# Kernel optimization log

Hardware: AMD Instinct MI355X
Metric: run time of the kernel (lower is better)

## Reference

```python
import jax, jax.numpy as jnp
import numpy as np

N, E, D = 50000, 1200000, 64
NEG_SLOPE = 0.2  # PyG GATConv LeakyReLU slope
EPS_SM = 1e-16   # PyG softmax eps
EPS_LN = 1e-5


def _glorot(key, shape):
    fan = shape[0]
    return jax.random.normal(key, shape, jnp.float32) / np.float32(np.sqrt(fan))


def setup_inputs() -> dict:
    key = jax.random.key(0)
    ks = jax.random.split(key, 16)
    inp = {
        "x": jax.random.normal(ks[0], (N, D), jnp.float32),
        "edge_index": jax.random.randint(ks[1], (2, E), 0, N, dtype=jnp.int32),
        # layer 0: bipartite-style (-1,-1) GATConv -> separate src/dst projections
        "W_src0": _glorot(ks[2], (D, D)), "W_dst0": _glorot(ks[3], (D, D)),
        "a_src0": _glorot(ks[4], (D,)), "a_dst0": _glorot(ks[5], (D,)),
        "b0": jnp.zeros((D,), jnp.float32),
        "lin_W0": _glorot(ks[6], (D, D)), "lin_b0": jnp.zeros((D,), jnp.float32),
        # layers 1,2: int in_channels -> shared projection for src and dst
        "W1": _glorot(ks[7], (D, D)),
        "a_src1": _glorot(ks[8], (D,)), "a_dst1": _glorot(ks[9], (D,)),
        "b1": jnp.zeros((D,), jnp.float32),
        "lin_W1": _glorot(ks[10], (D, D)), "lin_b1": jnp.zeros((D,), jnp.float32),
        "W2": _glorot(ks[11], (D, D)),
        "a_src2": _glorot(ks[12], (D,)), "a_dst2": _glorot(ks[13], (D,)),
        "b2": jnp.zeros((D,), jnp.float32),
        "lin_W2": _glorot(ks[14], (D, D)), "lin_b2": jnp.zeros((D,), jnp.float32),
        "ln_w": jnp.ones((D,), jnp.float32), "ln_b": jnp.zeros((D,), jnp.float32),
        "proj_W": _glorot(ks[15], (D, 1)), "proj_b": jnp.zeros((1,), jnp.float32),
    }
    return inp


def _gat(x_src, x_dst, a_src, a_dst, bias, src, dst):
    # per-edge attention logit: a_src.x_j + a_dst.x_i, LeakyReLU
    alpha = (x_src * a_src).sum(-1)[src] + (x_dst * a_dst).sum(-1)[dst]  # [E]
    alpha = jnp.where(alpha >= 0, alpha, NEG_SLOPE * alpha)
    # segment softmax over edges sharing a destination node
    m = jax.ops.segment_max(alpha, dst, num_segments=N)
    m = jnp.where(jnp.isfinite(m), m, 0.0)  # empty segments -> -inf -> 0
    e = jnp.exp(alpha - m[dst])
    denom = jax.ops.segment_sum(e, dst, num_segments=N)
    w = e / (denom[dst] + EPS_SM)
    # weighted scatter-add aggregation
    return jax.ops.segment_sum(w[:, None] * x_src[src], dst, num_segments=N) + bias


def reference(x, edge_index,
              W_src0, W_dst0, a_src0, a_dst0, b0, lin_W0, lin_b0,
              W1, a_src1, a_dst1, b1, lin_W1, lin_b1,
              W2, a_src2, a_dst2, b2, lin_W2, lin_b2,
              ln_w, ln_b, proj_W, proj_b):
    src, dst = edge_index[0], edge_index[1]
    h = _gat(x @ W_src0, x @ W_dst0, a_src0, a_dst0, b0, src, dst) + x @ lin_W0 + lin_b0
    h = jax.nn.relu(h)
    hp = h @ W1
    h = _gat(hp, hp, a_src1, a_dst1, b1, src, dst) + h @ lin_W1 + lin_b1
    h = jax.nn.relu(h)
    hp = h @ W2
    h = _gat(hp, hp, a_src2, a_dst2, b2, src, dst) + h @ lin_W2 + lin_b2
    # PyG LayerNorm mode='graph': normalize over all nodes and channels
    mu = h.mean()
    var = h.var()
    h = (h - mu) * jax.lax.rsqrt(var + EPS_LN) * ln_w + ln_b
    return h @ proj_W + proj_b  # [N, 1]
```

## Files before the change

kernel.cpp:

```cpp
#include <hip/hip_runtime.h>
#include <hip/hip_bf16.h>

#define NN 50000
#define NE 1200000
#define D 64
#define NEG_SLOPE 0.2f
#define EPS_SM 1e-16f
#define EPS_LN 1e-5f
#define KMAX 4
#define PIPE 8
#define BSH 6
#define NBUK 782
#define BCAP 2048
#define BCAPSH 11
#define EPB 4096
#define NPB 293
#define PACKB 48
#define GEMM_BLOCKS 3125
#define GAT_BLOCKS 12500

typedef __attribute__((ext_vector_type(8))) short short8;
typedef __attribute__((ext_vector_type(4))) float float4v;

__device__ __forceinline__ float waveReduceSum(float v) {
    #pragma unroll
    for (int off = 32; off > 0; off >>= 1)
        v += __shfl_xor(v, off, 64);
    return v;
}
__device__ __forceinline__ float bflo(unsigned v) { return __uint_as_float(v << 16); }
__device__ __forceinline__ float bfhi(unsigned v) { return __uint_as_float(v & 0xffff0000u); }
__device__ __forceinline__ short f2bf_bits(float f) {
    __hip_bfloat16 b = __float2bfloat16(f);
    short v; __builtin_memcpy(&v, &b, 2);
    return v;
}

struct WP7 { const float* p[7]; };

__global__ __launch_bounds__(256) void prep(WP7 wp, unsigned short* __restrict__ wpk,
                                            const int* __restrict__ ei,
                                            int* __restrict__ bcur,
                                            int* __restrict__ pairs) {
    if (blockIdx.x >= NPB) {
        const int n = 7 * 4096;
        for (int idx = (blockIdx.x - NPB) * 256 + threadIdx.x; idx < n; idx += PACKB * 256) {
            const int j = idx & 7;
            const int lane = (idx >> 3) & 63;
            const int khtile = idx >> 9;
            const int kh = khtile & 1;
            const int tile = khtile >> 1;
            const int mat = tile >> 2;
            const int ch = (tile & 3) * 16 + (lane & 15);
            const int k = kh * 32 + (lane >> 4) * 8 + j;
            wpk[idx] = (unsigned short)f2bf_bits(wp.p[mat][k * D + ch]);
        }
        return;
    }
    __shared__ int h[NBUK];
    __shared__ int cur[NBUK];
    for (int i = threadIdx.x; i < NBUK; i += 256) h[i] = 0;
    __syncthreads();
    const int base = blockIdx.x * EPB;
    const int lim  = min(EPB, NE - base);
    for (int i = threadIdx.x; i < lim; i += 256)
        atomicAdd(&h[ei[NE + base + i] >> BSH], 1);
    __syncthreads();
    for (int i = threadIdx.x; i < NBUK; i += 256) {
        const int c = h[i];
        cur[i] = c ? atomicAdd(&bcur[i], c) : 0;
    }
    __syncthreads();
    for (int i = threadIdx.x; i < lim; i += 256) {
        const int s = ei[base + i];
        const int d = ei[NE + base + i];
        const int b = d >> BSH;
        const int pos = atomicAdd(&cur[b], 1);
        if (pos < BCAP) pairs[(b << BCAPSH) + pos] = s | ((d & 63) << 16);
    }
}

template <int NMATS>
__global__ __launch_bounds__(256) void gemm_mfma(
                          const float* __restrict__ hin,
                          const unsigned short* __restrict__ wpk,
                          const float* __restrict__ avs,
                          const float* __restrict__ avd,
                          const float* __restrict__ bgat,
                          const float* __restrict__ blin,
                          __hip_bfloat16* __restrict__ hp,
                          float* __restrict__ agg,
                          float* __restrict__ alpha_s,
                          float* __restrict__ alpha_d) {
    constexpr int NT   = NMATS * 4;
    constexpr int NTPW = NT / 4;
    __shared__ float ared[2][4][16];
    __shared__ unsigned short hpt[16][68];
    __shared__ float aggt[16][69];

    const int t   = threadIdx.x;
    const int nb0 = blockIdx.x * 16;

    const int w    = t >> 6;
    const int lane = t & 63;
    const int mrow = lane & 15;
    const int kq   = lane >> 4;

    const float* xrow = hin + (size_t)(nb0 + mrow) * D + kq * 8;
    short8 a[2];
    #pragma unroll
    for (int kh = 0; kh < 2; ++kh) {
        const float4 f0 = *(const float4*)(xrow + kh * 32);
        const float4 f1 = *(const float4*)(xrow + kh * 32 + 4);
        a[kh][0] = f2bf_bits(f0.x); a[kh][1] = f2bf_bits(f0.y);
        a[kh][2] = f2bf_bits(f0.z); a[kh][3] = f2bf_bits(f0.w);
        a[kh][4] = f2bf_bits(f1.x); a[kh][5] = f2bf_bits(f1.y);
        a[kh][6] = f2bf_bits(f1.z); a[kh][7] = f2bf_bits(f1.w);
    }

    float4v acc[NTPW];
    #pragma unroll
    for (int i = 0; i < NTPW; ++i) {
        const int tile = w * NTPW + i;
        const short8 b0 = *(const short8*)(wpk + ((size_t)(tile * 2 + 0) * 64 + lane) * 8);
        const short8 b1 = *(const short8*)(wpk + ((size_t)(tile * 2 + 1) * 64 + lane) * 8);
        float4v c = {0.f, 0.f, 0.f, 0.f};
        c = __builtin_amdgcn_mfma_f32_16x16x32_bf16(a[0], b0, c, 0, 0, 0);
        c = __builtin_amdgcn_mfma_f32_16x16x32_bf16(a[1], b1, c, 0, 0, 0);
        acc[i] = c;
    }

    float psr[4] = {0.f, 0.f, 0.f, 0.f};
    float pdr[4] = {0.f, 0.f, 0.f, 0.f};
    #pragma unroll
    for (int i = 0; i < NTPW; ++i) {
        const int tile = w * NTPW + i;
        const int mat  = tile >> 2;
        const int c64  = (tile & 3) * 16 + mrow;
        const float av_s = avs[c64], av_d = avd[c64];
        const float bias = blin[c64] + bgat[c64];
        #pragma unroll
        for (int r = 0; r < 4; ++r) {
            const int ln = kq * 4 + r;
            const float v = acc[i][r];
            if (mat == 0) {
                hpt[ln][c64] = (unsigned short)f2bf_bits(v);
                psr[r] += v * av_s;
                if (NMATS == 2) pdr[r] += v * av_d;
            } else if (NMATS == 3 && mat == 1) {
                pdr[r] += v * av_d;
            } else {
                aggt[ln][c64] = v + bias;
            }
        }
    }
    #pragma unroll
    for (int off = 1; off < 16; off <<= 1) {
        #pragma unroll
        for (int r = 0; r < 4; ++r) {
            psr[r] += __shfl_xor(psr[r], off, 64);
            pdr[r] += __shfl_xor(pdr[r], off, 64);
        }
    }
    if (mrow == 0) {
        #pragma unroll
        for (int r = 0; r < 4; ++r) {
            ared[0][w][kq * 4 + r] = psr[r];
            ared[1][w][kq * 4 + r] = pdr[r];
        }
    }
    __syncthreads();

    {
        const int row = t >> 4;
        const int c0  = (t & 15) * 4;
        const float4 av = { aggt[row][c0], aggt[row][c0 + 1],
                            aggt[row][c0 + 2], aggt[row][c0 + 3] };
        *(float4*)(agg + (size_t)(nb0 + row) * D + c0) = av;
    }
    if (t < 128) {
        const int hr = t >> 3;
        const int h0 = (t & 7) * 8;
        const unsigned* hrow = (const unsigned*)&hpt[hr][h0];
        const uint4 hv = { hrow[0], hrow[1], hrow[2], hrow[3] };
        *(uint4*)((unsigned short*)hp + (size_t)(nb0 + hr) * D + h0) = hv;
    }
    if (t < 16) {
        alpha_s[nb0 + t] = ared[0][0][t] + ared[0][1][t] + ared[0][2][t] + ared[0][3][t];
        alpha_d[nb0 + t] = ared[1][0][t] + ared[1][1][t] + ared[1][2][t] + ared[1][3][t];
    }
}

__global__ __launch_bounds__(256) void csr_finalize(const int* __restrict__ pairs,
                                                    const int* __restrict__ bcur,
                                                    int* __restrict__ cnt,
                                                    int* __restrict__ row_start,
                                                    int* __restrict__ csr_src) {
    __shared__ int ncnt[64];
    __shared__ int lsrc[BCAP];
    const int t = threadIdx.x;
    const int b = blockIdx.x;
    const int beg = b << BCAPSH;
    const int m = min(bcur[b], BCAP);
    const int nbase = b << BSH;
    if (t < 64) ncnt[t] = 0;
    __syncthreads();
    for (int i = t; i < m; i += 256)
        atomicAdd(&ncnt[pairs[beg + i] >> 16], 1);
    __syncthreads();
    if (t < 64) {
        const int v = ncnt[t];
        int inc = v;
        #pragma unroll
        for (int off = 1; off < 64; off <<= 1) {
            const int u = __shfl_up(inc, off, 64);
            if (t >= off) inc += u;
        }
        const int excl = inc - v;
        if (nbase + t < NN) {
            cnt[nbase + t] = v;
            row_start[nbase + t] = beg + excl;
        }
        ncnt[t] = excl;
    }
    __syncthreads();
    for (int i = t; i < m; i += 256) {
        const int p = pairs[beg + i];
        const int pos = atomicAdd(&ncnt[p >> 16], 1);
        lsrc[pos] = p & 0xffff;
    }
    __syncthreads();
    for (int i = t; i < m; i += 256)
        csr_src[beg + i] = lsrc[i];
}

template <bool DO_RELU, bool DO_STATS>
__global__ __launch_bounds__(256) void gat_node(
                         const int* __restrict__ csr_src,
                         const int* __restrict__ row_start,
                         const int* __restrict__ cnt,
                         const float* __restrict__ as,
                         const float* __restrict__ ad,
                         const __hip_bfloat16* __restrict__ hp,
                         float* __restrict__ agg,
                         float* __restrict__ partial) {
    __shared__ int2 esm[4][KMAX * 64];
    const int wv   = threadIdx.x >> 6;
    const int lane = threadIdx.x & 63;
    const int node = blockIdx.x * 4 + wv;
    const int snode = __builtin_amdgcn_readfirstlane(node);
    const int deg = cnt[snode];
    const int rs  = row_start[snode];
    const int half = lane >> 5;
    const int c2   = lane & 31;
    float2 acc = make_float2(0.f, 0.f);
    if (deg > 0) {
        const float ad_d = ad[snode];
        int   sr[KMAX];
        float ea[KMAX];
        float sum = 0.f;
        #pragma unroll
        for (int k = 0; k < KMAX; ++k) {
            const int j = k * 64 + lane;
            const bool valid = j < deg;
            const int s = valid ? __builtin_nontemporal_load(csr_src + rs + j) : 0;
            float a = valid ? (as[s] + ad_d) : 0.f;
            a = (a >= 0.f) ? a : NEG_SLOPE * a;
            float e = valid ? __expf(a) : 0.f;
            sr[k] = s;
            ea[k] = e;
            sum += e;
        }
        sum = waveReduceSum(sum);
        const float inv = 1.f / (sum + EPS_SM);
        #pragma unroll
        for (int k = 0; k < KMAX; ++k)
            esm[wv][k * 64 + lane] = make_int2(sr[k] * 32, __float_as_int(ea[k] * inv));
        const unsigned* hp32 = (const unsigned*)hp;
        const int T    = (deg + 1) >> 1;
        const int Tpad = (T + PIPE - 1) & ~(PIPE - 1);
        int2     pp[PIPE];
        unsigned vv[PIPE];
        #pragma unroll
        for (int i = 0; i < PIPE; ++i) {
            const int2 p = esm[wv][2 * i + half];
            pp[i] = p;
            vv[i] = hp32[p.x + c2];
        }
        float2 a0 = make_float2(0.f, 0.f), a1 = make_float2(0.f, 0.f);
        for (int t0 = 0; t0 + PIPE < Tpad; t0 += PIPE) {
            #pragma unroll
            for (int i = 0; i < PIPE; ++i) {
                const float    w = __int_as_float(pp[i].y);
                const unsigned v = vv[i];
                const int2 np = esm[wv][2 * (t0 + PIPE + i) + half];
                pp[i] = np;
                vv[i] = hp32[np.x + c2];
                if (i & 1) {
                    a1.x = fmaf(w, bflo(v), a1.x);
                    a1.y = fmaf(w, bfhi(v), a1.y);
                } else {
                    a0.x = fmaf(w, bflo(v), a0.x);
                    a0.y = fmaf(w, bfhi(v), a0.y);
                }
            }
        }
        #pragma unroll
        for (int i = 0; i < PIPE; ++i) {
            const float w = __int_as_float(pp[i].y);
            if (i & 1) {
                a1.x = fmaf(w, bflo(vv[i]), a1.x);
                a1.y = fmaf(w, bfhi(vv[i]), a1.y);
            } else {
                a0.x = fmaf(w, bflo(vv[i]), a0.x);
                a0.y = fmaf(w, bfhi(vv[i]), a0.y);
            }
        }
        acc.x = a0.x + a1.x;
        acc.y = a0.y + a1.y;
    }
    acc.x += __shfl_xor(acc.x, 32, 64);
    acc.y += __shfl_xor(acc.y, 32, 64);

    float2 r2 = make_float2(0.f, 0.f);
    if (half == 0) {
        const float2 g = *(const float2*)(agg + (size_t)node * D + 2 * c2);
        r2.x = g.x + acc.x;
        r2.y = g.y + acc.y;
        if (DO_RELU) { r2.x = fmaxf(r2.x, 0.f); r2.y = fmaxf(r2.y, 0.f); }
        *(float2*)(agg + (size_t)node * D + 2 * c2) = r2;
    }
    if (DO_STATS) {
        float s  = r2.x + r2.y;
        float ss = r2.x * r2.x + r2.y * r2.y;
        s  = waveReduceSum(s);
        ss = waveReduceSum(ss);
        __shared__ float red[2][4];
        if (lane == 0) { red[0][wv] = s; red[1][wv] = ss; }
        __syncthreads();
        if (threadIdx.x == 0) {
            partial[blockIdx.x]              = red[0][0] + red[0][1] + red[0][2] + red[0][3];
            partial[GAT_BLOCKS + blockIdx.x] = red[1][0] + red[1][1] + red[1][2] + red[1][3];
        }
    }
}

__global__ void ln_reduce(const float* __restrict__ partial, float* __restrict__ stats) {
    float s = 0.f, ss = 0.f;
    for (int i = threadIdx.x; i < GAT_BLOCKS; i += 256) {
        s  += partial[i];
        ss += partial[GAT_BLOCKS + i];
    }
    s  = waveReduceSum(s);
    ss = waveReduceSum(ss);
    __shared__ float sm[2][4];
    if ((threadIdx.x & 63) == 0) {
        sm[0][threadIdx.x >> 6] = s;
        sm[1][threadIdx.x >> 6] = ss;
    }
    __syncthreads();
    if (threadIdx.x == 0) {
        stats[0] = sm[0][0] + sm[0][1] + sm[0][2] + sm[0][3];
        stats[1] = sm[1][0] + sm[1][1] + sm[1][2] + sm[1][3];
    }
}

__global__ void finalize(const float* __restrict__ x,
                         const float* __restrict__ stats,
                         const float* __restrict__ lnw,
                         const float* __restrict__ lnb,
                         const float* __restrict__ pw,
                         const float* __restrict__ pb,
                         float* __restrict__ out) {
    const int wave = (blockIdx.x * blockDim.x + threadIdx.x) >> 6;
    const int lane = threadIdx.x & 63;
    if (wave >= NN) return;
    const float inv_nd = 1.f / (float)(NN * D);
    const float mu  = stats[0] * inv_nd;
    const float var = stats[1] * inv_nd - mu * mu;
    const float rs = rsqrtf(var + EPS_LN);
    const float v = x[(size_t)wave * D + lane];
    const float xn = (v - mu) * rs * lnw[lane] + lnb[lane];
    const float c = waveReduceSum(xn * pw[lane]);
    if (lane == 0) out[wave] = c + pb[0];
}

extern "C" void kernel_launch(void* const* d_in, const int* in_sizes, int n_in,
                              void* d_out, int out_size, void* d_ws, size_t ws_size,
                              hipStream_t stream) {
    const float* x     = (const float*)d_in[0];
    const int*   ei    = (const int*)d_in[1];
    const float* Wsrc0 = (const float*)d_in[2];
    const float* Wdst0 = (const float*)d_in[3];
    const float* asrc0 = (const float*)d_in[4];
    const float* adst0 = (const float*)d_in[5];
    const float* b0    = (const float*)d_in[6];
    const float* linW0 = (const float*)d_in[7];
    const float* linb0 = (const float*)d_in[8];
    const float* W1    = (const float*)d_in[9];
    const float* asrc1 = (const float*)d_in[10];
    const float* adst1 = (const float*)d_in[11];
    const float* b1    = (const float*)d_in[12];
    const float* linW1 = (const float*)d_in[13];
    const float* linb1 = (const float*)d_in[14];
    const float* W2    = (const float*)d_in[15];
    const float* asrc2 = (const float*)d_in[16];
    const float* adst2 = (const float*)d_in[17];
    const float* b2    = (const float*)d_in[18];
    const float* linW2 = (const float*)d_in[19];
    const float* linb2 = (const float*)d_in[20];
    const float* lnw   = (const float*)d_in[21];
    const float* lnb   = (const float*)d_in[22];
    const float* pW    = (const float*)d_in[23];
    const float* pb    = (const float*)d_in[24];
    float* out = (float*)d_out;

    int*  csr_src   = (int*)d_ws;
    int*  cnt       = csr_src + NBUK * BCAP;
    int*  row_start = cnt + NN;
    int*  bcur      = row_start + NN;
    size_t off = (size_t)(NBUK * BCAP + 2 * NN + NBUK);
    off = (off + 3) & ~(size_t)3;
    float* A     = (float*)d_ws + off;
    int*   pairs = (int*)A;
    float* B     = A + (size_t)NN * D;
    __hip_bfloat16* P = (__hip_bfloat16*)(B + NN * D);
    float* alpha_s = (float*)(P + NN * D);
    float* alpha_d = alpha_s + NN;
    float* stats   = alpha_d + NN;
    float* partial = stats + 2;
    unsigned short* wpk = (unsigned short*)(((uintptr_t)(partial + 2 * GAT_BLOCKS) + 15) & ~(uintptr_t)15);

    const int elem_blocks = (NN * D) / 256;

    WP7 wp = {{Wsrc0, Wdst0, linW0, W1, linW1, W2, linW2}};
    hipMemsetAsync(bcur, 0, NBUK * sizeof(int), stream);
    prep<<<NPB + PACKB, 256, 0, stream>>>(wp, wpk, ei, bcur, pairs);
    csr_finalize<<<NBUK, 256, 0, stream>>>(pairs, bcur, cnt, row_start, csr_src);

    gemm_mfma<3><<<GEMM_BLOCKS, 256, 0, stream>>>(x, wpk, asrc0, adst0, b0, linb0,
                                                  P, A, alpha_s, alpha_d);
    gat_node<true, false><<<GAT_BLOCKS, 256, 0, stream>>>(csr_src, row_start, cnt,
                                                          alpha_s, alpha_d, P, A, partial);

    gemm_mfma<2><<<GEMM_BLOCKS, 256, 0, stream>>>(A, wpk + 3 * 4096, asrc1, adst1, b1, linb1,
                                                  P, B, alpha_s, alpha_d);
    gat_node<true, false><<<GAT_BLOCKS, 256, 0, stream>>>(csr_src, row_start, cnt,
                                                          alpha_s, alpha_d, P, B, partial);

    gemm_mfma<2><<<GEMM_BLOCKS, 256, 0, stream>>>(B, wpk + 5 * 4096, asrc2, adst2, b2, linb2,
                                                  P, A, alpha_s, alpha_d);
    gat_node<false, true><<<GAT_BLOCKS, 256, 0, stream>>>(csr_src, row_start, cnt,
                                                          alpha_s, alpha_d, P, A, partial);

    ln_reduce<<<1, 256, 0, stream>>>(partial, stats);
    finalize<<<elem_blocks, 256, 0, stream>>>(A, stats, lnw, lnb, pW, pb, out);
}
```

Measured before the change: 313.1 us.

## Fuse all stages into one cooperative persistent kernel with grid syncs

Replaces the chain of separate kernel launches (prep, CSR finalize, three GEMM+GAT layer pairs, LN reduce, finalize) with a single persistent cooperative kernel of 512 blocks that loops over the virtual blocks of each phase and separates phases with grid.sync. The LayerNorm statistics reduction is changed from a per-block partial array plus a reduce kernel to atomic adds into 8 striped accumulators, zeroed by the existing memset. This targets launch overhead and inter-kernel gaps, but limits occupancy to the persistent grid and adds grid-wide barrier costs. A fallback to the multi-kernel path is kept when cooperative launch is unavailable.

```diff
diff --git a/kernel.cpp b/kernel.cpp
--- a/kernel.cpp
+++ b/kernel.cpp
@@ -1,5 +1,8 @@
 #include <hip/hip_runtime.h>
 #include <hip/hip_bf16.h>
+#include <hip/hip_cooperative_groups.h>
+
+namespace cg = cooperative_groups;
 
 #define NN 50000
 #define NE 1200000
@@ -18,6 +21,8 @@
 #define PACKB 48
 #define GEMM_BLOCKS 3125
 #define GAT_BLOCKS 12500
+#define GRID 512
+#define NTHREADS 256
 
 typedef __attribute__((ext_vector_type(8))) short short8;
 typedef __attribute__((ext_vector_type(4))) float float4v;
@@ -37,6 +42,7 @@
 }
 
 struct WP7 { const float* p[7]; };
+
 
 __global__ __launch_bounds__(256) void prep(WP7 wp, unsigned short* __restrict__ wpk,
                                             const int* __restrict__ ei,
@@ -92,15 +98,13 @@
                           float* __restrict__ agg,
                           float* __restrict__ alpha_s,
                           float* __restrict__ alpha_d) {
-    constexpr int NT   = NMATS * 4;
-    constexpr int NTPW = NT / 4;
+    constexpr int NTPW = NMATS;
     __shared__ float ared[2][4][16];
     __shared__ unsigned short hpt[16][68];
     __shared__ float aggt[16][69];
 
     const int t   = threadIdx.x;
     const int nb0 = blockIdx.x * 16;
-
     const int w    = t >> 6;
     const int lane = t & 63;
     const int mrow = lane & 15;
@@ -170,7 +174,6 @@
         }
     }
     __syncthreads();
-
     {
         const int row = t >> 4;
         const int c0  = (t & 15) * 4;
@@ -243,7 +246,7 @@
                          const float* __restrict__ ad,
                          const __hip_bfloat16* __restrict__ hp,
                          float* __restrict__ agg,
-                         float* __restrict__ partial) {
+                         float* __restrict__ stats) {
     __shared__ int2 esm[4][KMAX * 64];
     const int wv   = threadIdx.x >> 6;
     const int lane = threadIdx.x & 63;
@@ -339,29 +342,9 @@
         if (lane == 0) { red[0][wv] = s; red[1][wv] = ss; }
         __syncthreads();
         if (threadIdx.x == 0) {
-            partial[blockIdx.x]              = red[0][0] + red[0][1] + red[0][2] + red[0][3];
-            partial[GAT_BLOCKS + blockIdx.x] = red[1][0] + red[1][1] + red[1][2] + red[1][3];
-        }
-    }
-}
-
-__global__ void ln_reduce(const float* __restrict__ partial, float* __restrict__ stats) {
-    float s = 0.f, ss = 0.f;
-    for (int i = threadIdx.x; i < GAT_BLOCKS; i += 256) {
-        s  += partial[i];
-        ss += partial[GAT_BLOCKS + i];
-    }
-    s  = waveReduceSum(s);
-    ss = waveReduceSum(ss);
-    __shared__ float sm[2][4];
-    if ((threadIdx.x & 63) == 0) {
-        sm[0][threadIdx.x >> 6] = s;
-        sm[1][threadIdx.x >> 6] = ss;
-    }
-    __syncthreads();
-    if (threadIdx.x == 0) {
-        stats[0] = sm[0][0] + sm[0][1] + sm[0][2] + sm[0][3];
-        stats[1] = sm[1][0] + sm[1][1] + sm[1][2] + sm[1][3];
+            atomicAdd(&stats[blockIdx.x & 7],       red[0][0] + red[0][1] + red[0][2] + red[0][3]);
+            atomicAdd(&stats[8 + (blockIdx.x & 7)], red[1][0] + red[1][1] + red[1][2] + red[1][3]);
+        }
     }
 }
 
@@ -375,9 +358,12 @@
     const int wave = (blockIdx.x * blockDim.x + threadIdx.x) >> 6;
     const int lane = threadIdx.x & 63;
     if (wave >= NN) return;
+    float s = 0.f, ss = 0.f;
+    #pragma unroll
+    for (int i = 0; i < 8; ++i) { s += stats[i]; ss += stats[8 + i]; }
     const float inv_nd = 1.f / (float)(NN * D);
-    const float mu  = stats[0] * inv_nd;
-    const float var = stats[1] * inv_nd - mu * mu;
+    const float mu  = s * inv_nd;
+    const float var = ss * inv_nd - mu * mu;
     const float rs = rsqrtf(var + EPS_LN);
     const float v = x[(size_t)wave * D + lane];
     const float xn = (v - mu) * rs * lnw[lane] + lnb[lane];
@@ -385,41 +371,378 @@
     if (lane == 0) out[wave] = c + pb[0];
 }
 
+
+struct MegaArgs {
+    const float* x;
+    const int*   ei;
+    const float* wp[7];
+    const float* avs[3]; const float* avd[3];
+    const float* bg[3];  const float* bl[3];
+    const float* lnw; const float* lnb; const float* pW; const float* pb;
+    float* out;
+    int* csr_src; int* cnt; int* row_start; int* bcur; int* pairs;
+    float* A; float* B; __hip_bfloat16* P;
+    float* alpha_s; float* alpha_d; float* stats;
+    unsigned short* wpk;
+};
+
+template <int NMATS>
+__device__ void gemm_phase(const float* hin, const unsigned short* wpk,
+                           const float* avs, const float* avd,
+                           const float* bgat, const float* blin,
+                           __hip_bfloat16* hp, float* agg,
+                           float* alpha_s, float* alpha_d, char* smraw) {
+    constexpr int NTPW = NMATS;
+    float* ared          = (float*)smraw;
+    float* aggt          = (float*)(smraw + 512);
+    unsigned short* hpt  = (unsigned short*)(smraw + 512 + 4416);
+
+    const int t    = threadIdx.x;
+    const int w    = t >> 6;
+    const int lane = t & 63;
+    const int mrow = lane & 15;
+    const int kq   = lane >> 4;
+
+    for (int vb = blockIdx.x; vb < GEMM_BLOCKS; vb += GRID) {
+        __syncthreads();
+        const int nb0 = vb * 16;
+        const float* xrow = hin + (size_t)(nb0 + mrow) * D + kq * 8;
+        short8 a[2];
+        #pragma unroll
+        for (int kh = 0; kh < 2; ++kh) {
+            const float4 f0 = *(const float4*)(xrow + kh * 32);
+            const float4 f1 = *(const float4*)(xrow + kh * 32 + 4);
+            a[kh][0] = f2bf_bits(f0.x); a[kh][1] = f2bf_bits(f0.y);
+            a[kh][2] = f2bf_bits(f0.z); a[kh][3] = f2bf_bits(f0.w);
+            a[kh][4] = f2bf_bits(f1.x); a[kh][5] = f2bf_bits(f1.y);
+            a[kh][6] = f2bf_bits(f1.z); a[kh][7] = f2bf_bits(f1.w);
+        }
+        float4v acc[NTPW];
+        #pragma unroll
+        for (int i = 0; i < NTPW; ++i) {
+            const int tile = w * NTPW + i;
+            const short8 b0 = *(const short8*)(wpk + ((size_t)(tile * 2 + 0) * 64 + lane) * 8);
+            const short8 b1 = *(const short8*)(wpk + ((size_t)(tile * 2 + 1) * 64 + lane) * 8);
+            float4v c = {0.f, 0.f, 0.f, 0.f};
+            c = __builtin_amdgcn_mfma_f32_16x16x32_bf16(a[0], b0, c, 0, 0, 0);
+            c = __builtin_amdgcn_mfma_f32_16x16x32_bf16(a[1], b1, c, 0, 0, 0);
+            acc[i] = c;
+        }
+        float psr[4] = {0.f, 0.f, 0.f, 0.f};
+        float pdr[4] = {0.f, 0.f, 0.f, 0.f};
+        #pragma unroll
+        for (int i = 0; i < NTPW; ++i) {
+            const int tile = w * NTPW + i;
+            const int mat  = tile >> 2;
+            const int c64  = (tile & 3) * 16 + mrow;
+            const float av_s = avs[c64], av_d = avd[c64];
+            const float bias = blin[c64] + bgat[c64];
+            #pragma unroll
+            for (int r = 0; r < 4; ++r) {
+                const int ln = kq * 4 + r;
+                const float v = acc[i][r];
+                if (mat == 0) {
+                    hpt[ln * 68 + c64] = (unsigned short)f2bf_bits(v);
+                    psr[r] += v * av_s;
+                    if (NMATS == 2) pdr[r] += v * av_d;
+                } else if (NMATS == 3 && mat == 1) {
+                    pdr[r] += v * av_d;
+                } else {
+                    aggt[ln * 69 + c64] = v + bias;
+                }
+            }
+        }
+        #pragma unroll
+        for (int off = 1; off < 16; off <<= 1) {
+            #pragma unroll
+            for (int r = 0; r < 4; ++r) {
+                psr[r] += __shfl_xor(psr[r], off, 64);
+                pdr[r] += __shfl_xor(pdr[r], off, 64);
+            }
+        }
+        if (mrow == 0) {
+            #pragma unroll
+            for (int r = 0; r < 4; ++r) {
+                ared[(0 * 4 + w) * 16 + kq * 4 + r] = psr[r];
+                ared[(1 * 4 + w) * 16 + kq * 4 + r] = pdr[r];
+            }
+        }
+        __syncthreads();
+        {
+            const int row = t >> 4;
+            const int c0  = (t & 15) * 4;
+            const float4 av = { aggt[row * 69 + c0],     aggt[row * 69 + c0 + 1],
+                                aggt[row * 69 + c0 + 2], aggt[row * 69 + c0 + 3] };
+            *(float4*)(agg + (size_t)(nb0 + row) * D + c0) = av;
+        }
+        if (t < 128) {
+            const int hr = t >> 3;
+            const int h0 = (t & 7) * 8;
+            const unsigned* hrow = (const unsigned*)&hpt[hr * 68 + h0];
+            const uint4 hv = { hrow[0], hrow[1], hrow[2], hrow[3] };
+            *(uint4*)((unsigned short*)hp + (size_t)(nb0 + hr) * D + h0) = hv;
+        }
+        if (t < 16) {
+            alpha_s[nb0 + t] = ared[0 * 16 + t] + ared[1 * 16 + t]
+                             + ared[2 * 16 + t] + ared[3 * 16 + t];
+            alpha_d[nb0 + t] = ared[4 * 16 + t] + ared[5 * 16 + t]
+                             + ared[6 * 16 + t] + ared[7 * 16 + t];
+        }
+    }
+}
+
+__device__ void gat_phase(const int* csr_src, const int* row_start, const int* cnt,
+                          const float* as, const float* ad, const __hip_bfloat16* hp,
+                          float* agg, float* stats,
+                          bool do_relu, bool do_stats, char* smraw) {
+    __shared__ float gred[8];
+    int2* esm = (int2*)smraw;
+    const int wv   = threadIdx.x >> 6;
+    const int lane = threadIdx.x & 63;
+    const int half = lane >> 5;
+    const int c2   = lane & 31;
+    int2* esw = esm + wv * (KMAX * 64);
+    float accS = 0.f, accSS = 0.f;
+
+    for (int vb = blockIdx.x; vb < GAT_BLOCKS; vb += GRID) {
+        const int node = vb * 4 + wv;
+        const int snode = __builtin_amdgcn_readfirstlane(node);
+        const int deg = cnt[snode];
+        const int rs  = row_start[snode];
+        float2 acc = make_float2(0.f, 0.f);
+        if (deg > 0) {
+            const float ad_d = ad[snode];
+            int   sr[KMAX];
+            float ea[KMAX];
+            float sum = 0.f;
+            #pragma unroll
+            for (int k = 0; k < KMAX; ++k) {
+                const int j = k * 64 + lane;
+                const bool valid = j < deg;
+                const int s = valid ? __builtin_nontemporal_load(csr_src + rs + j) : 0;
+                float aa = valid ? (as[s] + ad_d) : 0.f;
+                aa = (aa >= 0.f) ? aa : NEG_SLOPE * aa;
+                float e = valid ? __expf(aa) : 0.f;
+                sr[k] = s;
+                ea[k] = e;
+                sum += e;
+            }
+            sum = waveReduceSum(sum);
+            const float inv = 1.f / (sum + EPS_SM);
+            #pragma unroll
+            for (int k = 0; k < KMAX; ++k)
+                esw[k * 64 + lane] = make_int2(sr[k] * 32, __float_as_int(ea[k] * inv));
+            const unsigned* hp32 = (const unsigned*)hp;
+            const int T    = (deg + 1) >> 1;
+            const int Tpad = (T + PIPE - 1) & ~(PIPE - 1);
+            int2     pp[PIPE];
+            unsigned vv[PIPE];
+            #pragma unroll
+            for (int i = 0; i < PIPE; ++i) {
+                const int2 p = esw[2 * i + half];
+                pp[i] = p;
+                vv[i] = hp32[p.x + c2];
+            }
+            float2 a0 = make_float2(0.f, 0.f), a1 = make_float2(0.f, 0.f);
+            for (int t0 = 0; t0 + PIPE < Tpad; t0 += PIPE) {
+                #pragma unroll
+                for (int i = 0; i < PIPE; ++i) {
+                    const float    w = __int_as_float(pp[i].y);
+                    const unsigned v = vv[i];
+                    const int2 np = esw[2 * (t0 + PIPE + i) + half];
+                    pp[i] = np;
+                    vv[i] = hp32[np.x + c2];
+                    if (i & 1) {
+                        a1.x = fmaf(w, bflo(v), a1.x);
+                        a1.y = fmaf(w, bfhi(v), a1.y);
+                    } else {
+                        a0.x = fmaf(w, bflo(v), a0.x);
+                        a0.y = fmaf(w, bfhi(v), a0.y);
+                    }
+                }
+            }
+            #pragma unroll
+            for (int i = 0; i < PIPE; ++i) {
+                const float w = __int_as_float(pp[i].y);
+                if (i & 1) {
+                    a1.x = fmaf(w, bflo(vv[i]), a1.x);
+                    a1.y = fmaf(w, bfhi(vv[i]), a1.y);
+                } else {
+                    a0.x = fmaf(w, bflo(vv[i]), a0.x);
+                    a0.y = fmaf(w, bfhi(vv[i]), a0.y);
+                }
+            }
+            acc.x = a0.x + a1.x;
+            acc.y = a0.y + a1.y;
+        }
+        acc.x += __shfl_xor(acc.x, 32, 64);
+        acc.y += __shfl_xor(acc.y, 32, 64);
+
+        float2 r2 = make_float2(0.f, 0.f);
+        if (half == 0) {
+            const float2 g = *(const float2*)(agg + (size_t)node * D + 2 * c2);
+            r2.x = g.x + acc.x;
+            r2.y = g.y + acc.y;
+            if (do_relu) { r2.x = fmaxf(r2.x, 0.f); r2.y = fmaxf(r2.y, 0.f); }
+            *(float2*)(agg + (size_t)node * D + 2 * c2) = r2;
+        }
+        if (do_stats) {
+            float s1 = r2.x + r2.y;
+            float s2 = r2.x * r2.x + r2.y * r2.y;
+            accS  += waveReduceSum(s1);
+            accSS += waveReduceSum(s2);
+        }
+    }
+    if (do_stats) {
+        __syncthreads();
+        if (lane == 0) { gred[wv] = accS; gred[4 + wv] = accSS; }
+        __syncthreads();
+        if (threadIdx.x == 0) {
+            atomicAdd(&stats[blockIdx.x & 7],       gred[0] + gred[1] + gred[2] + gred[3]);
+            atomicAdd(&stats[8 + (blockIdx.x & 7)], gred[4] + gred[5] + gred[6] + gred[7]);
+        }
+    }
+}
+
+__global__ __launch_bounds__(NTHREADS, 2) void mega(MegaArgs a) {
+    cg::grid_group grid = cg::this_grid();
+    __shared__ __align__(16) char smraw[8192];
+    __shared__ int ncnt[64];
+
+    const int t   = threadIdx.x;
+    const int bid = blockIdx.x;
+    const int g   = bid * NTHREADS + t;
+
+    for (int idx = g; idx < 7 * 4096; idx += GRID * NTHREADS) {
+        const int j = idx & 7;
+        const int lane = (idx >> 3) & 63;
+        const int khtile = idx >> 9;
+        const int kh = khtile & 1;
+        const int tile = khtile >> 1;
+        const int mat = tile >> 2;
+        const int ch = (tile & 3) * 16 + (lane & 15);
+        const int k = kh * 32 + (lane >> 4) * 8 + j;
+        a.wpk[idx] = (unsigned short)f2bf_bits(a.wp[mat][k * D + ch]);
+    }
+    if (bid < NPB) {
+        int* h   = (int*)smraw;
+        int* cur = h + NBUK;
+        for (int i = t; i < NBUK; i += NTHREADS) h[i] = 0;
+        __syncthreads();
+        const int base = bid * EPB;
+        const int lim  = min(EPB, NE - base);
+        for (int i = t; i < lim; i += NTHREADS)
+            atomicAdd(&h[a.ei[NE + base + i] >> BSH], 1);
+        __syncthreads();
+        for (int i = t; i < NBUK; i += NTHREADS) {
+            const int c = h[i];
+            cur[i] = c ? atomicAdd(&a.bcur[i], c) : 0;
+        }
+        __syncthreads();
+        for (int i = t; i < lim; i += NTHREADS) {
+            const int s = a.ei[base + i];
+            const int d = a.ei[NE + base + i];
+            const int b = d >> BSH;
+            const int pos = atomicAdd(&cur[b], 1);
+            if (pos < BCAP) a.pairs[(b << BCAPSH) + pos] = s | ((d & 63) << 16);
+        }
+    }
+    grid.sync();
+
+    for (int b = bid; b < NBUK; b += GRID) {
+        __syncthreads();
+        int* lsrc = (int*)smraw;
+        const int beg = b << BCAPSH;
+        const int m = min(a.bcur[b], BCAP);
+        const int nbase = b << BSH;
+        if (t < 64) ncnt[t] = 0;
+        __syncthreads();
+        for (int i = t; i < m; i += NTHREADS)
+            atomicAdd(&ncnt[a.pairs[beg + i] >> 16], 1);
+        __syncthreads();
+        if (t < 64) {
+            const int v = ncnt[t];
+            int inc = v;
+            #pragma unroll
+            for (int off = 1; off < 64; off <<= 1) {
+                const int u = __shfl_up(inc, off, 64);
+                if (t >= off) inc += u;
+            }
+            const int excl = inc - v;
+            if (nbase + t < NN) {
+                a.cnt[nbase + t] = v;
+                a.row_start[nbase + t] = beg + excl;
+            }
+            ncnt[t] = excl;
+        }
+        __syncthreads();
+        for (int i = t; i < m; i += NTHREADS) {
+            const int p = a.pairs[beg + i];
+            const int pos = atomicAdd(&ncnt[p >> 16], 1);
+            lsrc[pos] = p & 0xffff;
+        }
+        __syncthreads();
+        for (int i = t; i < m; i += NTHREADS)
+            a.csr_src[beg + i] = lsrc[i];
+    }
+    grid.sync();
+
+    gemm_phase<3>(a.x, a.wpk, a.avs[0], a.avd[0], a.bg[0], a.bl[0],
+                  a.P, a.A, a.alpha_s, a.alpha_d, smraw);
+    grid.sync();
+    gat_phase(a.csr_src, a.row_start, a.cnt, a.alpha_s, a.alpha_d,
+              a.P, a.A, a.stats, true, false, smraw);
+    grid.sync();
+
+    gemm_phase<2>(a.A, a.wpk + 3 * 4096, a.avs[1], a.avd[1], a.bg[1], a.bl[1],
+                  a.P, a.B, a.alpha_s, a.alpha_d, smraw);
+    grid.sync();
+    gat_phase(a.csr_src, a.row_start, a.cnt, a.alpha_s, a.alpha_d,
+              a.P, a.B, a.stats, true, false, smraw);
+    grid.sync();
+
+    gemm_phase<2>(a.B, a.wpk + 5 * 4096, a.avs[2], a.avd[2], a.bg[2], a.bl[2],
+                  a.P, a.A, a.alpha_s, a.alpha_d, smraw);
+    grid.sync();
+    gat_phase(a.csr_src, a.row_start, a.cnt, a.alpha_s, a.alpha_d,
+              a.P, a.A, a.stats, false, true, smraw);
+    grid.sync();
+
+    {
+        const int wv   = t >> 6;
+        const int lane = t & 63;
+        float s = 0.f, ss = 0.f;
+        #pragma unroll
+        for (int i = 0; i < 8; ++i) { s += a.stats[i]; ss += a.stats[8 + i]; }
+        const float inv_nd = 1.f / (float)(NN * D);
+        const float mu  = s * inv_nd;
+        const float var = ss * inv_nd - mu * mu;
+        const float rs = rsqrtf(var + EPS_LN);
+        const float lw = a.lnw[lane], lb = a.lnb[lane], pw = a.pW[lane];
+        const float pbv = a.pb[0];
+        for (int vb = bid; vb < GAT_BLOCKS; vb += GRID) {
+            const int node = vb * 4 + wv;
+            const float v = a.A[(size_t)node * D + lane];
+            const float xn = (v - mu) * rs * lw + lb;
+            const float c = waveReduceSum(xn * pw);
+            if (lane == 0) a.out[node] = c + pbv;
+        }
+    }
+}
+
 extern "C" void kernel_launch(void* const* d_in, const int* in_sizes, int n_in,
                               void* d_out, int out_size, void* d_ws, size_t ws_size,
                               hipStream_t stream) {
     const float* x     = (const float*)d_in[0];
     const int*   ei    = (const int*)d_in[1];
-    const float* Wsrc0 = (const float*)d_in[2];
-    const float* Wdst0 = (const float*)d_in[3];
-    const float* asrc0 = (const float*)d_in[4];
-    const float* adst0 = (const float*)d_in[5];
-    const float* b0    = (const float*)d_in[6];
-    const float* linW0 = (const float*)d_in[7];
-    const float* linb0 = (const float*)d_in[8];
-    const float* W1    = (const float*)d_in[9];
-    const float* asrc1 = (const float*)d_in[10];
-    const float* adst1 = (const float*)d_in[11];
-    const float* b1    = (const float*)d_in[12];
-    const float* linW1 = (const float*)d_in[13];
-    const float* linb1 = (const float*)d_in[14];
-    const float* W2    = (const float*)d_in[15];
-    const float* asrc2 = (const float*)d_in[16];
-    const float* adst2 = (const float*)d_in[17];
-    const float* b2    = (const float*)d_in[18];
-    const float* linW2 = (const float*)d_in[19];
-    const float* linb2 = (const float*)d_in[20];
-    const float* lnw   = (const float*)d_in[21];
-    const float* lnb   = (const float*)d_in[22];
-    const float* pW    = (const float*)d_in[23];
-    const float* pb    = (const float*)d_in[24];
     float* out = (float*)d_out;
 
     int*  csr_src   = (int*)d_ws;
     int*  cnt       = csr_src + NBUK * BCAP;
     int*  row_start = cnt + NN;
     int*  bcur      = row_start + NN;
-    size_t off = (size_t)(NBUK * BCAP + 2 * NN + NBUK);
+    float* stats    = (float*)(bcur + NBUK);
+    size_t off = (size_t)(NBUK * BCAP + 2 * NN + NBUK + 16);
     off = (off + 3) & ~(size_t)3;
     float* A     = (float*)d_ws + off;
     int*   pairs = (int*)A;
@@ -427,32 +750,63 @@
     __hip_bfloat16* P = (__hip_bfloat16*)(B + NN * D);
     float* alpha_s = (float*)(P + NN * D);
     float* alpha_d = alpha_s + NN;
-    float* stats   = alpha_d + NN;
-    float* partial = stats + 2;
-    unsigned short* wpk = (unsigned short*)(((uintptr_t)(partial + 2 * GAT_BLOCKS) + 15) & ~(uintptr_t)15);
-
-    const int elem_blocks = (NN * D) / 256;
-
-    WP7 wp = {{Wsrc0, Wdst0, linW0, W1, linW1, W2, linW2}};
-    hipMemsetAsync(bcur, 0, NBUK * sizeof(int), stream);
-    prep<<<NPB + PACKB, 256, 0, stream>>>(wp, wpk, ei, bcur, pairs);
-    csr_finalize<<<NBUK, 256, 0, stream>>>(pairs, bcur, cnt, row_start, csr_src);
-
-    gemm_mfma<3><<<GEMM_BLOCKS, 256, 0, stream>>>(x, wpk, asrc0, adst0, b0, linb0,
-                                                  P, A, alpha_s, alpha_d);
-    gat_node<true, false><<<GAT_BLOCKS, 256, 0, stream>>>(csr_src, row_start, cnt,
-                                                          alpha_s, alpha_d, P, A, partial);
-
-    gemm_mfma<2><<<GEMM_BLOCKS, 256, 0, stream>>>(A, wpk + 3 * 4096, asrc1, adst1, b1, linb1,
-                                                  P, B, alpha_s, alpha_d);
-    gat_node<true, false><<<GAT_BLOCKS, 256, 0, stream>>>(csr_src, row_start, cnt,
-                                                          alpha_s, alpha_d, P, B, partial);
-
-    gemm_mfma<2><<<GEMM_BLOCKS, 256, 0, stream>>>(B, wpk + 5 * 4096, asrc2, adst2, b2, linb2,
-                                                  P, A, alpha_s, alpha_d);
-    gat_node<false, true><<<GAT_BLOCKS, 256, 0, stream>>>(csr_src, row_start, cnt,
-                                                          alpha_s, alpha_d, P, A, partial);
-
-    ln_reduce<<<1, 256, 0, stream>>>(partial, stats);
-    finalize<<<elem_blocks, 256, 0, stream>>>(A, stats, lnw, lnb, pW, pb, out);
-}
+    unsigned short* wpk = (unsigned short*)(((uintptr_t)(alpha_d + NN) + 15) & ~(uintptr_t)15);
+
+    hipMemsetAsync(bcur, 0, (NBUK + 16) * sizeof(int), stream);
+
+    MegaArgs a;
+    a.x = x; a.ei = ei;
+    a.wp[0] = (const float*)d_in[2];   a.wp[1] = (const float*)d_in[3];
+    a.wp[2] = (const float*)d_in[7];   a.wp[3] = (const float*)d_in[9];
+    a.wp[4] = (const float*)d_in[13];  a.wp[5] = (const float*)d_in[15];
+    a.wp[6] = (const float*)d_in[19];
+    a.avs[0] = (const float*)d_in[4];  a.avd[0] = (const float*)d_in[5];
+    a.bg[0]  = (const float*)d_in[6];  a.bl[0]  = (const float*)d_in[8];
+    a.avs[1] = (const float*)d_in[10]; a.avd[1] = (const float*)d_in[11];
+    a.bg[1]  = (const float*)d_in[12]; a.bl[1]  = (const float*)d_in[14];
+    a.avs[2] = (const float*)d_in[16]; a.avd[2] = (const float*)d_in[17];
+    a.bg[2]  = (const float*)d_in[18]; a.bl[2]  = (const float*)d_in[20];
+    a.lnw = (const float*)d_in[21]; a.lnb = (const float*)d_in[22];
+    a.pW  = (const float*)d_in[23]; a.pb  = (const float*)d_in[24];
+    a.out = out;
+    a.csr_src = csr_src; a.cnt = cnt; a.row_start = row_start;
+    a.bcur = bcur; a.pairs = pairs;
+    a.A = A; a.B = B; a.P = P;
+    a.alpha_s = alpha_s; a.alpha_d = alpha_d; a.stats = stats;
+    a.wpk = wpk;
+
+    bool coop_ok = false;
+    int dev = 0;
+    if (hipGetDevice(&dev) == hipSuccess) {
+        int attr = 0;
+        if (hipDeviceGetAttribute(&attr, hipDeviceAttributeCooperativeLaunch, dev) == hipSuccess && attr) {
+            void* params[] = { &a };
+            coop_ok = (hipLaunchCooperativeKernel((const void*)mega, dim3(GRID), dim3(NTHREADS),
+                                                  params, 0, stream) == hipSuccess);
+            if (!coop_ok) (void)hipGetLastError();
+        }
+    }
+
+    if (!coop_ok) {
+        WP7 wp = {{a.wp[0], a.wp[1], a.wp[2], a.wp[3], a.wp[4], a.wp[5], a.wp[6]}};
+        prep<<<NPB + PACKB, 256, 0, stream>>>(wp, wpk, ei, bcur, pairs);
+        csr_finalize<<<NBUK, 256, 0, stream>>>(pairs, bcur, cnt, row_start, csr_src);
+
+        gemm_mfma<3><<<GEMM_BLOCKS, 256, 0, stream>>>(x, wpk, a.avs[0], a.avd[0], a.bg[0], a.bl[0],
+                                                      P, A, alpha_s, alpha_d);
+        gat_node<true, false><<<GAT_BLOCKS, 256, 0, stream>>>(csr_src, row_start, cnt,
+                                                              alpha_s, alpha_d, P, A, stats);
+
+        gemm_mfma<2><<<GEMM_BLOCKS, 256, 0, stream>>>(A, wpk + 3 * 4096, a.avs[1], a.avd[1], a.bg[1], a.bl[1],
+                                                      P, B, alpha_s, alpha_d);
+        gat_node<true, false><<<GAT_BLOCKS, 256, 0, stream>>>(csr_src, row_start, cnt,
+                                                              alpha_s, alpha_d, P, B, stats);
+
+        gemm_mfma<2><<<GEMM_BLOCKS, 256, 0, stream>>>(B, wpk + 5 * 4096, a.avs[2], a.avd[2], a.bg[2], a.bl[2],
+                                                      P, A, alpha_s, alpha_d);
+        gat_node<false, true><<<GAT_BLOCKS, 256, 0, stream>>>(csr_src, row_start, cnt,
+                                                              alpha_s, alpha_d, P, A, stats);
+
+        finalize<<<(NN * D) / 256, 256, 0, stream>>>(A, stats, a.lnw, a.lnb, a.pW, a.pb, out);
+    }
+}
```

Result: slower. 912.9 us (+191.6%).
